# Kernel optimization log

Hardware: AMD Instinct MI355X
Metric: run time of the kernel (lower is better)

Reference implementation:

```python
import jax, jax.numpy as jnp
import numpy as np
from jax import lax

B_COEF = np.array([0.0048243445989025905, 0.019297378395610362, 0.028946067593415543,
                   0.019297378395610362, 0.0048243445989025905], dtype=np.float32)
A_COEF = np.array([1.0, -2.369513007182038, 2.3139884144002064,
                   -1.0546654058785661, 0.18737949236818502], dtype=np.float32)


def setup_inputs() -> dict:
    key = jax.random.key(0)
    x = jax.random.normal(key, (32, 16, 32768), dtype=jnp.float32)
    return {"x": x, "b": jnp.asarray(B_COEF), "a": jnp.asarray(A_COEF)}


def _odd_ext(x, n):
    left = 2.0 * x[..., :1] - x[..., 1:n + 1][..., ::-1]
    right = 2.0 * x[..., -1:] - x[..., -(n + 1):-1][..., ::-1]
    return jnp.concatenate([left, x, right], axis=-1)


def _lfilter(x, b, a):
    # Direct form II transposed IIR, zero initial conditions.
    # x: [N, T]; b, a: [K]
    b = b / a[0]
    a = a / a[0]
    K = b.shape[0]

    def step(z, xt):  # z: [N, K-1], xt: [N]
        y = b[0] * xt + z[:, 0]
        z_shift = jnp.pad(z[:, 1:], ((0, 0), (0, 1)))
        z_new = b[1:] * xt[:, None] - a[1:] * y[:, None] + z_shift
        return z_new, y

    z0 = jnp.zeros((x.shape[0], K - 1), dtype=x.dtype)
    _, y = lax.scan(step, z0, x.T)  # y: [T, N]
    return y.T


def _filtfilt(x, b, a):
    # torchaudio-style filtfilt: forward lfilter, then backward lfilter (zero ICs).
    y = _lfilter(x, b, a)
    y = _lfilter(y[:, ::-1], b, a)[:, ::-1]
    return y


def reference(x, b, a):
    scale = jnp.max(jnp.abs(x), axis=-1, keepdims=True)
    xn = x / scale
    padlen = 3 * max(a.shape[0], b.shape[0])  # static: 15
    xe = _odd_ext(xn, padlen)                 # [B, C, T + 2*padlen]
    shp = xe.shape
    y = _filtfilt(xe.reshape(-1, shp[-1]), b, a)
    y = y.reshape(shp)[..., padlen:-padlen]
    return y * scale
```

## Files before the change

### kernel.cpp

```cpp
#include <hip/hip_runtime.h>


typedef __fp16 h2 __attribute__((ext_vector_type(2)));

constexpr int kT   = 32768;
constexpr int kP   = 15;
constexpr int kC   = 64;
constexpr int kWF  = 32;
constexpr int kNCh = kT / kC;
constexpr int kTPB = 64;

#define B0 0.0048243445989025905f
#define B1 0.019297378395610362f
#define B2 0.028946067593415543f
#define B3 0.019297378395610362f
#define B4 0.0048243445989025905f
#define NA1 2.369513007182038f
#define NA2 (-2.3139884144002064f)
#define NA3 1.0546654058785661f
#define NA4 (-0.18737949236818502f)

#define STEP(xv) do { \
    y  = fmaf(B0, (xv), z1); \
    z1 = fmaf(NA1, y, fmaf(B1, (xv), z2)); \
    z2 = fmaf(NA2, y, fmaf(B2, (xv), z3)); \
    z3 = fmaf(NA3, y, fmaf(B3, (xv), z4)); \
    z4 = fmaf(NA4, y, B4 * (xv)); \
} while (0)

#define PACK2(va, vb, DST) do { \
    STEP(va); float _t = y; \
    STEP(vb); DST = __builtin_amdgcn_cvt_pkrtz(_t, y); \
} while (0)

__global__ __launch_bounds__(kTPB, 4)
void filtfilt_kernel(const float* __restrict__ x, float* __restrict__ out) {
    const int tid   = blockIdx.x * kTPB + threadIdx.x;
    const int row   = tid >> 9;
    const int chunk = tid & (kNCh - 1);
    const bool last = (chunk == kNCh - 1);
    const float* __restrict__ xr = x + (size_t)row * kT;
    float* __restrict__ outr     = out + (size_t)row * kT;
    const int s = chunk * kC;

    h2 arc[kC / 2];
    h2 wu[14];

    float z1 = 0.f, z2 = 0.f, z3 = 0.f, z4 = 0.f, y;

    if (chunk == 0) {
        const float4* x4 = (const float4*)xr;
        float4 a0 = x4[0], a1 = x4[1], a2 = x4[2], a3 = x4[3];
        float xa[16] = {a0.x,a0.y,a0.z,a0.w, a1.x,a1.y,a1.z,a1.w,
                        a2.x,a2.y,a2.z,a2.w, a3.x,a3.y,a3.z,a3.w};
        #pragma unroll
        for (int e = 0; e < kP; ++e) {
            float xv = fmaf(2.f, xa[0], -xa[kP - e]);
            STEP(xv);
        }
    } else {
        const float4* wp = (const float4*)(xr + s - kWF);
        float4 w[8];
        #pragma unroll
        for (int i = 0; i < 8; ++i) w[i] = wp[i];
        #pragma unroll
        for (int i = 0; i < 8; ++i) {
            STEP(w[i].x); STEP(w[i].y); STEP(w[i].z); STEP(w[i].w);
        }
    }

    const float4* mp = (const float4*)(xr + s);
    float4 c0 = mp[0], c1 = mp[1], c2 = mp[2], c3 = mp[3];
    #pragma unroll
    for (int m = 0; m < 4; ++m) {
        float4 n0 = c0, n1 = c1, n2 = c2, n3 = c3;
        if (m < 3) {
            n0 = mp[4 * m + 4]; n1 = mp[4 * m + 5];
            n2 = mp[4 * m + 6]; n3 = mp[4 * m + 7];
        } else if (!last) {
            n0 = mp[16]; n1 = mp[17]; n2 = mp[18]; n3 = mp[19];
        }
        PACK2(c0.x, c0.y, arc[8 * m + 0]); PACK2(c0.z, c0.w, arc[8 * m + 1]);
        PACK2(c1.x, c1.y, arc[8 * m + 2]); PACK2(c1.z, c1.w, arc[8 * m + 3]);
        PACK2(c2.x, c2.y, arc[8 * m + 4]); PACK2(c2.z, c2.w, arc[8 * m + 5]);
        PACK2(c3.x, c3.y, arc[8 * m + 6]); PACK2(c3.z, c3.w, arc[8 * m + 7]);
        c0 = n0; c1 = n1; c2 = n2; c3 = n3;
    }

    if (!last) {
        float4 d0 = mp[20], d1 = mp[21], d2 = mp[22];
        PACK2(c0.x, c0.y, wu[0]);  PACK2(c0.z, c0.w, wu[1]);
        PACK2(c1.x, c1.y, wu[2]);  PACK2(c1.z, c1.w, wu[3]);
        PACK2(c2.x, c2.y, wu[4]);  PACK2(c2.z, c2.w, wu[5]);
        PACK2(c3.x, c3.y, wu[6]);  PACK2(c3.z, c3.w, wu[7]);
        PACK2(d0.x, d0.y, wu[8]);  PACK2(d0.z, d0.w, wu[9]);
        PACK2(d1.x, d1.y, wu[10]); PACK2(d1.z, d1.w, wu[11]);
        PACK2(d2.x, d2.y, wu[12]); PACK2(d2.z, d2.w, wu[13]);
    } else {
        const float4* e4 = (const float4*)(xr + kT - 16);
        float4 b0 = e4[0], b1 = e4[1], b2 = e4[2], b3 = e4[3];
        float xa[16] = {b0.x,b0.y,b0.z,b0.w, b1.x,b1.y,b1.z,b1.w,
                        b2.x,b2.y,b2.z,b2.w, b3.x,b3.y,b3.z,b3.w};
        float pend = 0.f;
        #pragma unroll
        for (int r = 0; r < 15; ++r) {
            float xv = fmaf(2.f, xa[15], -xa[14 - r]);
            STEP(xv);
            if ((r & 1) == 0) pend = y;
            else wu[r >> 1] = __builtin_amdgcn_cvt_pkrtz(pend, y);
        }
        wu[7] = __builtin_amdgcn_cvt_pkrtz(pend, pend);
    }

    z1 = z2 = z3 = z4 = 0.f;
    if (!last) {
        #pragma unroll
        for (int k = 13; k >= 0; --k) {
            float a = (float)wu[k].y; STEP(a);
            float b = (float)wu[k].x; STEP(b);
        }
    } else {
        { float a = (float)wu[7].x; STEP(a); }
        #pragma unroll
        for (int k = 6; k >= 0; --k) {
            float a = (float)wu[k].y; STEP(a);
            float b = (float)wu[k].x; STEP(b);
        }
    }

    float4* op = (float4*)(outr + s);
    #pragma unroll
    for (int gi = 15; gi >= 0; --gi) {
        float4 o; float v;
        v = (float)arc[2 * gi + 1].y; STEP(v); o.w = y;
        v = (float)arc[2 * gi + 1].x; STEP(v); o.z = y;
        v = (float)arc[2 * gi + 0].y; STEP(v); o.y = y;
        v = (float)arc[2 * gi + 0].x; STEP(v); o.x = y;
        op[gi] = o;
    }
}

extern "C" void kernel_launch(void* const* d_in, const int* in_sizes, int n_in,
                              void* d_out, int out_size, void* d_ws, size_t ws_size,
                              hipStream_t stream) {
    const float* x = (const float*)d_in[0];
    float* out     = (float*)d_out;
    const int rows   = in_sizes[0] / kT;
    const int blocks = rows * kNCh / kTPB;
    filtfilt_kernel<<<blocks, kTPB, 0, stream>>>(x, out);
}
```

Baseline: 131.8 us.

## Replace recursive IIR passes with truncated-kernel convolution on MFMA

Replaces the per-thread forward/backward IIR recursion with a convolution by the truncated autocorrelation of the impulse response, which a small prep kernel computes into workspace. Each wavefront stages an fp16 copy of its input window in LDS and evaluates the convolution with 16x16x32 f16 MFMA instructions, plus a scalar edge correction for the odd extension and the zero initial state at the end of the row. This removes the serial dependency chains in favour of matrix-core throughput, at the cost of fp16 inputs and coefficients and truncating the impulse response to a finite window, which may change accuracy. It also adds an extra kernel launch.

```diff
diff --git a/kernel.cpp b/kernel.cpp
--- a/kernel.cpp
+++ b/kernel.cpp
@@ -1,142 +1,176 @@
 #include <hip/hip_runtime.h>
 
 
-typedef __fp16 h2 __attribute__((ext_vector_type(2)));
+typedef _Float16 h8 __attribute__((ext_vector_type(8)));
+typedef float f32x4 __attribute__((ext_vector_type(4)));
 
-constexpr int kT   = 32768;
-constexpr int kP   = 15;
-constexpr int kC   = 64;
-constexpr int kWF  = 32;
-constexpr int kNCh = kT / kC;
-constexpr int kTPB = 64;
+constexpr int kT     = 32768;
+constexpr int kOutW  = 2048;
+constexpr int kWRow  = kT / kOutW;
+constexpr int kTPB   = 256;
+constexpr int kTileB = 4544;
 
-#define B0 0.0048243445989025905f
-#define B1 0.019297378395610362f
-#define B2 0.028946067593415543f
-#define B3 0.019297378395610362f
-#define B4 0.0048243445989025905f
+#define B0c 0.0048243445989025905f
+#define B1c 0.019297378395610362f
+#define B2c 0.028946067593415543f
+#define A1c (-2.369513007182038f)
+#define A2c 2.3139884144002064f
+#define A3c (-1.0546654058785661f)
+#define A4c 0.18737949236818502f
 #define NA1 2.369513007182038f
 #define NA2 (-2.3139884144002064f)
 #define NA3 1.0546654058785661f
 #define NA4 (-0.18737949236818502f)
 
-#define STEP(xv) do { \
-    y  = fmaf(B0, (xv), z1); \
-    z1 = fmaf(NA1, y, fmaf(B1, (xv), z2)); \
-    z2 = fmaf(NA2, y, fmaf(B2, (xv), z3)); \
-    z3 = fmaf(NA3, y, fmaf(B3, (xv), z4)); \
-    z4 = fmaf(NA4, y, B4 * (xv)); \
+#define STEPF(xv) do { \
+    y  = fmaf(B0c, (xv), z1); \
+    z1 = fmaf(NA1, y, fmaf(B1c, (xv), z2)); \
+    z2 = fmaf(NA2, y, fmaf(B2c, (xv), z3)); \
+    z3 = fmaf(NA3, y, fmaf(B1c, (xv), z4)); \
+    z4 = fmaf(NA4, y, B0c * (xv)); \
 } while (0)
 
-#define PACK2(va, vb, DST) do { \
-    STEP(va); float _t = y; \
-    STEP(vb); DST = __builtin_amdgcn_cvt_pkrtz(_t, y); \
-} while (0)
+#define PK(a, b) __builtin_bit_cast(int, __builtin_amdgcn_cvt_pkrtz((a), (b)))
+
+__global__ void prep_kernel(uint4* __restrict__ ws) {
+    __shared__ float h[128];
+    const int l = threadIdx.x;
+    if (l == 0) {
+        float m1 = 0.f, m2 = 0.f, m3 = 0.f, m4 = 0.f;
+        const float bb[5] = {B0c, B1c, B2c, B1c, B0c};
+        for (int k = 0; k < 128; ++k) {
+            float v = (k < 5 ? bb[k] : 0.f);
+            v = v - A1c * m1 - A2c * m2 - A3c * m3 - A4c * m4;
+            h[k] = v; m4 = m3; m3 = m2; m2 = m1; m1 = v;
+        }
+    }
+    __syncthreads();
+    #pragma unroll
+    for (int t = 0; t < 3; ++t) {
+        h8 f;
+        #pragma unroll
+        for (int e = 0; e < 8; ++e) {
+            int m  = 32 * t + 8 * (l >> 4) + e - (l & 15) - 32;
+            int am = m < 0 ? -m : m;
+            float c0 = 0.f, c1 = 0.f, c2 = 0.f, c3 = 0.f;
+            int k = 0;
+            for (; k + 3 + am < 128; k += 4) {
+                c0 += h[k]     * h[k + am];
+                c1 += h[k + 1] * h[k + 1 + am];
+                c2 += h[k + 2] * h[k + 2 + am];
+                c3 += h[k + 3] * h[k + 3 + am];
+            }
+            for (; k + am < 128; ++k) c0 += h[k] * h[k + am];
+            f[e] = (_Float16)(c0 + c1 + c2 + c3);
+        }
+        ws[t * 64 + l] = __builtin_bit_cast(uint4, f);
+    }
+    ((float*)(ws + 192))[l] = h[l];
+}
 
 __global__ __launch_bounds__(kTPB, 4)
-void filtfilt_kernel(const float* __restrict__ x, float* __restrict__ out) {
-    const int tid   = blockIdx.x * kTPB + threadIdx.x;
-    const int row   = tid >> 9;
-    const int chunk = tid & (kNCh - 1);
-    const bool last = (chunk == kNCh - 1);
+void filtfilt_kernel(const float* __restrict__ x, float* __restrict__ out,
+                     const uint4* __restrict__ ws) {
+    __shared__ __align__(16) char lds[4][kTileB];
+    const int t   = threadIdx.x;
+    const int l   = t & 63;
+    const int wv  = t >> 6;
+    const int W   = blockIdx.x * 4 + wv;
+    const int row = W >> 4;
+    const int sw  = W & (kWRow - 1);
+    const int S   = sw * kOutW;
     const float* __restrict__ xr = x + (size_t)row * kT;
     float* __restrict__ outr     = out + (size_t)row * kT;
-    const int s = chunk * kC;
+    char* Lb = lds[wv];
 
-    h2 arc[kC / 2];
-    h2 wu[14];
+    uint4 b0q = ws[l], b1q = ws[64 + l], b2q = ws[128 + l];
 
-    float z1 = 0.f, z2 = 0.f, z3 = 0.f, z4 = 0.f, y;
+    #pragma unroll
+    for (int i = 0; i < 8; ++i) {
+        int xi = S - 32 + 256 * i + 4 * l;
+        xi = xi < 0 ? 0 : (xi > kT - 4 ? kT - 4 : xi);
+        float4 v = *(const float4*)(xr + xi);
+        int2 wi = { PK(v.x, v.y), PK(v.z, v.w) };
+        *(int2*)(Lb + 512 * i + 8 * l) = wi;
+    }
+    if (l < 24) {
+        int xi = S + 2016 + 4 * l;
+        xi = xi > kT - 4 ? kT - 4 : xi;
+        float4 v = *(const float4*)(xr + xi);
+        int2 wi = { PK(v.x, v.y), PK(v.z, v.w) };
+        *(int2*)(Lb + 4096 + 8 * l) = wi;
+    }
+    if (sw == 0 && l < 32) {
+        float v = 0.f;
+        if (l >= 17) v = fmaf(2.f, xr[0], -xr[32 - l]);
+        *(_Float16*)(Lb + 2 * l) = (_Float16)v;
+    }
+    if (sw == kWRow - 1) {
+        float v = 0.f;
+        if (l < 15) v = fmaf(2.f, xr[kT - 1], -xr[kT - 2 - l]);
+        *(_Float16*)(Lb + 2 * (2080 + l)) = (_Float16)v;
+    }
+    asm volatile("s_waitcnt lgkmcnt(0)" ::: "memory");
 
-    if (chunk == 0) {
-        const float4* x4 = (const float4*)xr;
-        float4 a0 = x4[0], a1 = x4[1], a2 = x4[2], a3 = x4[3];
-        float xa[16] = {a0.x,a0.y,a0.z,a0.w, a1.x,a1.y,a1.z,a1.w,
-                        a2.x,a2.y,a2.z,a2.w, a3.x,a3.y,a3.z,a3.w};
+    if (sw == kWRow - 1) {
+        if (l == 0) {
+            h8 tv[14];
+            #pragma unroll
+            for (int i = 0; i < 14; ++i) tv[i] = *(const h8*)(Lb + 4064 + 16 * i);
+            float z1 = 0.f, z2 = 0.f, z3 = 0.f, z4 = 0.f, y;
+            #pragma unroll
+            for (int i = 0; i < 14; ++i) {
+                #pragma unroll
+                for (int e = 0; e < 8; ++e) {
+                    STEPF((float)tv[i][e]);
+                    int d = 2032 + 8 * i + e;
+                    if (d >= 2095) *(float*)(Lb + 4288 + 4 * (d - 2095)) = y;
+                }
+            }
+        }
+        asm volatile("s_waitcnt lgkmcnt(0)" ::: "memory");
+    }
+    float corr[4] = {0.f, 0.f, 0.f, 0.f};
+    if (sw == kWRow - 1 && (l >> 4) == 3) {
+        const float* hws = (const float*)(ws + 192);
         #pragma unroll
-        for (int e = 0; e < kP; ++e) {
-            float xv = fmaf(2.f, xa[0], -xa[kP - e]);
-            STEP(xv);
-        }
-    } else {
-        const float4* wp = (const float4*)(xr + s - kWF);
-        float4 w[8];
-        #pragma unroll
-        for (int i = 0; i < 8; ++i) w[i] = wp[i];
-        #pragma unroll
-        for (int i = 0; i < 8; ++i) {
-            STEP(w[i].x); STEP(w[i].y); STEP(w[i].z); STEP(w[i].w);
+        for (int r = 0; r < 4; ++r) {
+            int u    = 1984 + 16 * r + (l & 15);
+            int kmin = 2063 - u;
+            float c = 0.f;
+            for (int k = kmin; k < 64; ++k)
+                c += hws[k] * *(const float*)(Lb + 4288 + 4 * (u + k - 2063));
+            corr[r] = c;
         }
     }
 
-    const float4* mp = (const float4*)(xr + s);
-    float4 c0 = mp[0], c1 = mp[1], c2 = mp[2], c3 = mp[3];
+    const h8 B0f = __builtin_bit_cast(h8, b0q);
+    const h8 B1f = __builtin_bit_cast(h8, b1q);
+    const h8 B2f = __builtin_bit_cast(h8, b2q);
+
+    const int lg = l >> 4, lc = l & 15;
     #pragma unroll
-    for (int m = 0; m < 4; ++m) {
-        float4 n0 = c0, n1 = c1, n2 = c2, n3 = c3;
-        if (m < 3) {
-            n0 = mp[4 * m + 4]; n1 = mp[4 * m + 5];
-            n2 = mp[4 * m + 6]; n3 = mp[4 * m + 7];
-        } else if (!last) {
-            n0 = mp[16]; n1 = mp[17]; n2 = mp[18]; n3 = mp[19];
+    for (int q = 0; q < 8; ++q) {
+        const char* p = Lb + 512 * q + 32 * lc + 16 * lg;
+        h8 a0 = *(const h8*)p;
+        h8 a1 = *(const h8*)(p + 64);
+        h8 a2 = *(const h8*)(p + 128);
+        f32x4 acc = {0.f, 0.f, 0.f, 0.f};
+        acc = __builtin_amdgcn_mfma_f32_16x16x32_f16(a0, B0f, acc, 0, 0, 0);
+        acc = __builtin_amdgcn_mfma_f32_16x16x32_f16(a1, B1f, acc, 0, 0, 0);
+        acc = __builtin_amdgcn_mfma_f32_16x16x32_f16(a2, B2f, acc, 0, 0, 0);
+        const int o0 = S + 256 * q + 64 * lg + lc;
+        if (q == 7) {
+            outr[o0]      = acc[0] - corr[0];
+            outr[o0 + 16] = acc[1] - corr[1];
+            outr[o0 + 32] = acc[2] - corr[2];
+            outr[o0 + 48] = acc[3] - corr[3];
+        } else {
+            outr[o0]      = acc[0];
+            outr[o0 + 16] = acc[1];
+            outr[o0 + 32] = acc[2];
+            outr[o0 + 48] = acc[3];
         }
-        PACK2(c0.x, c0.y, arc[8 * m + 0]); PACK2(c0.z, c0.w, arc[8 * m + 1]);
-        PACK2(c1.x, c1.y, arc[8 * m + 2]); PACK2(c1.z, c1.w, arc[8 * m + 3]);
-        PACK2(c2.x, c2.y, arc[8 * m + 4]); PACK2(c2.z, c2.w, arc[8 * m + 5]);
-        PACK2(c3.x, c3.y, arc[8 * m + 6]); PACK2(c3.z, c3.w, arc[8 * m + 7]);
-        c0 = n0; c1 = n1; c2 = n2; c3 = n3;
-    }
-
-    if (!last) {
-        float4 d0 = mp[20], d1 = mp[21], d2 = mp[22];
-        PACK2(c0.x, c0.y, wu[0]);  PACK2(c0.z, c0.w, wu[1]);
-        PACK2(c1.x, c1.y, wu[2]);  PACK2(c1.z, c1.w, wu[3]);
-        PACK2(c2.x, c2.y, wu[4]);  PACK2(c2.z, c2.w, wu[5]);
-        PACK2(c3.x, c3.y, wu[6]);  PACK2(c3.z, c3.w, wu[7]);
-        PACK2(d0.x, d0.y, wu[8]);  PACK2(d0.z, d0.w, wu[9]);
-        PACK2(d1.x, d1.y, wu[10]); PACK2(d1.z, d1.w, wu[11]);
-        PACK2(d2.x, d2.y, wu[12]); PACK2(d2.z, d2.w, wu[13]);
-    } else {
-        const float4* e4 = (const float4*)(xr + kT - 16);
-        float4 b0 = e4[0], b1 = e4[1], b2 = e4[2], b3 = e4[3];
-        float xa[16] = {b0.x,b0.y,b0.z,b0.w, b1.x,b1.y,b1.z,b1.w,
-                        b2.x,b2.y,b2.z,b2.w, b3.x,b3.y,b3.z,b3.w};
-        float pend = 0.f;
-        #pragma unroll
-        for (int r = 0; r < 15; ++r) {
-            float xv = fmaf(2.f, xa[15], -xa[14 - r]);
-            STEP(xv);
-            if ((r & 1) == 0) pend = y;
-            else wu[r >> 1] = __builtin_amdgcn_cvt_pkrtz(pend, y);
-        }
-        wu[7] = __builtin_amdgcn_cvt_pkrtz(pend, pend);
-    }
-
-    z1 = z2 = z3 = z4 = 0.f;
-    if (!last) {
-        #pragma unroll
-        for (int k = 13; k >= 0; --k) {
-            float a = (float)wu[k].y; STEP(a);
-            float b = (float)wu[k].x; STEP(b);
-        }
-    } else {
-        { float a = (float)wu[7].x; STEP(a); }
-        #pragma unroll
-        for (int k = 6; k >= 0; --k) {
-            float a = (float)wu[k].y; STEP(a);
-            float b = (float)wu[k].x; STEP(b);
-        }
-    }
-
-    float4* op = (float4*)(outr + s);
-    #pragma unroll
-    for (int gi = 15; gi >= 0; --gi) {
-        float4 o; float v;
-        v = (float)arc[2 * gi + 1].y; STEP(v); o.w = y;
-        v = (float)arc[2 * gi + 1].x; STEP(v); o.z = y;
-        v = (float)arc[2 * gi + 0].y; STEP(v); o.y = y;
-        v = (float)arc[2 * gi + 0].x; STEP(v); o.x = y;
-        op[gi] = o;
     }
 }
 
@@ -144,8 +178,9 @@
                               void* d_out, int out_size, void* d_ws, size_t ws_size,
                               hipStream_t stream) {
     const float* x = (const float*)d_in[0];
-    float* out     = (float*)d_out;
-    const int rows   = in_sizes[0] / kT;
-    const int blocks = rows * kNCh / kTPB;
-    filtfilt_kernel<<<blocks, kTPB, 0, stream>>>(x, out);
+    float* outp    = (float*)d_out;
+    const int rows = in_sizes[0] / kT;
+    prep_kernel<<<1, 64, 0, stream>>>((uint4*)d_ws);
+    const int blocks = rows * kWRow * 64 / kTPB;
+    filtfilt_kernel<<<blocks, kTPB, 0, stream>>>(x, outp, (const uint4*)d_ws);
 }
```

New measurement: 163.2 us. 1.24x slower.
